# Performance work log

Measured on AMD Instinct MI355X. Metric: run time of the kernel, lower is better.

Reference implementation:

```python
import jax, jax.numpy as jnp
import numpy as np

DIM_IN = 16
DIM_OUT = 64

def setup_inputs() -> dict:
    key = jax.random.key(0)
    ks = jax.random.split(key, 7)
    B, T, N = 4, 8, 256
    s_in = 1.0 / np.sqrt(DIM_IN)
    s_out = 1.0 / np.sqrt(DIM_OUT)
    return {
        "query": jax.random.normal(ks[0], (B, N, DIM_IN), dtype=jnp.float32),
        "keys": jax.random.normal(ks[1], (B, T, N, DIM_IN), dtype=jnp.float32),
        "Wq": jax.random.uniform(ks[2], (DIM_IN, DIM_OUT), jnp.float32, -s_in, s_in),
        "bq": jax.random.uniform(ks[3], (DIM_OUT,), jnp.float32, -s_in, s_in),
        "Wk": jax.random.uniform(ks[4], (DIM_IN, DIM_OUT), jnp.float32, -s_in, s_in),
        "bk": jax.random.uniform(ks[5], (DIM_OUT,), jnp.float32, -s_in, s_in),
        "wt": jax.random.uniform(ks[6], (DIM_OUT,), jnp.float32, -s_out, s_out),
    }

def reference(query, keys, Wq, bq, Wk, bk, wt):
    # q: [B, N, D] -> [B, 1, N, 1, D]
    q = (jnp.einsum('bnf,fd->bnd', query, Wq) + bq)[:, None, :, None, :]
    # k: [B, T, N, D] -> [B, T, 1, N, D]
    k = (jnp.einsum('btnf,fd->btnd', keys, Wk) + bk)[:, :, None, :, :]
    # scores: [B, T, N, N] via tanh of broadcast add, reduced by wt
    scores = jnp.einsum('btnmd,d->btnm', jnp.tanh(q + k), wt)
    return jax.nn.softmax(scores, axis=-1)
```

## Files before the change

kernel.cpp:

```cpp
#include <hip/hip_runtime.h>

#define B_ 4
#define T_ 8
#define N_ 256
#define F_ 16
#define D_ 64
#define NP (D_/2)
#define CHUNK 8
#define NCH (N_/CHUNK)

#define SC 2.8853900817779268f
#define LOG2E 1.4426950408889634f

typedef __attribute__((ext_vector_type(16))) float f32x16;

__device__ __forceinline__ float fast_exp2(float x) { return __builtin_amdgcn_exp2f(x); }
__device__ __forceinline__ float fast_rcp(float x)  { return __builtin_amdgcn_rcpf(x); }

__global__ __launch_bounds__(256)
void tattn_proj_kernel(const float* __restrict__ query,
                       const float* __restrict__ keys,
                       const float* __restrict__ Wq, const float* __restrict__ bq,
                       const float* __restrict__ Wk, const float* __restrict__ bk,
                       float* __restrict__ Eq, float* __restrict__ Ek)
{
    const int tid = threadIdx.x;
    const int row = blockIdx.x * 4 + (tid >> 6);
    const int j   = tid & 63;
    const int NQ  = B_ * N_;

    if (row < NQ) {
        const float* in = query + (size_t)row * F_;
        float acc = bq[j];
        #pragma unroll
        for (int f = 0; f < F_; ++f) acc = fmaf(in[f], Wq[f * D_ + j], acc);
        Eq[(size_t)row * D_ + j] = fast_exp2(acc * SC);
    } else {
        const int r = row - NQ;
        const float* in = keys + (size_t)r * F_;
        float acc = bk[j];
        #pragma unroll
        for (int f = 0; f < F_; ++f) acc = fmaf(in[f], Wk[f * D_ + j], acc);
        Ek[(size_t)r * D_ + j] = fast_exp2(acc * SC);
    }
}

__global__ __launch_bounds__(256, 3)
void tattn_main_kernel(const float* __restrict__ Eq,
                       const float* __restrict__ Ek,
                       const float* __restrict__ wt,
                       float* __restrict__ out)
{
    __shared__ float pbuf[CHUNK][N_];
    __shared__ float wls[D_];
    __shared__ float totL[CHUNK];

    const int tid = threadIdx.x;
    const int bid = blockIdx.x;
    const int ch  = bid % NCH;
    const int t   = (bid / NCH) % T_;
    const int b   = bid / (NCH * T_);
    const int n0  = ch * CHUNK;

    if (tid < D_) wls[tid] = 2.0f * wt[tid];

    float kreg[D_];
    {
        const float* kp = Ek + (((size_t)(b * T_ + t)) * N_ + tid) * D_;
        #pragma unroll
        for (int d = 0; d < D_; d += 4) {
            float4 v = *reinterpret_cast<const float4*>(kp + d);
            kreg[d] = v.x; kreg[d+1] = v.y; kreg[d+2] = v.z; kreg[d+3] = v.w;
        }
    }
    __syncthreads();

    float wv[D_];
    #pragma unroll
    for (int d = 0; d < D_; d += 4) {
        float4 v = *reinterpret_cast<const float4*>(&wls[d]);
        wv[d] = v.x; wv[d+1] = v.y; wv[d+2] = v.z; wv[d+3] = v.w;
    }
    float Wsum = 0.f;
    #pragma unroll
    for (int d = 0; d < D_; ++d) Wsum += wv[d];
    Wsum *= 0.5f;

    const float* eqrow = Eq + ((size_t)(b * N_ + n0)) * D_;

    #pragma unroll 1
    for (int nn = 0; nn < CHUNK; ++nn) {
        f32x16 e0, e1, e2, e3;
        asm volatile("s_load_dwordx16 %0, %4, 0x0\n\t"
                     "s_load_dwordx16 %1, %4, 0x40\n\t"
                     "s_load_dwordx16 %2, %4, 0x80\n\t"
                     "s_load_dwordx16 %3, %4, 0xc0"
                     : "=&s"(e0), "=&s"(e1), "=&s"(e2), "=&s"(e3)
                     : "s"(eqrow));
        asm volatile("s_waitcnt lgkmcnt(0)"
                     : "+s"(e0), "+s"(e1), "+s"(e2), "+s"(e3));
        __builtin_amdgcn_sched_barrier(0);

        float a0 = 0.f, a1 = 0.f, a2 = 0.f, a3 = 0.f;
        #pragma unroll
        for (int pr = 0; pr < NP; ++pr) {
            float eqa, eqb;
            if      (pr <  8) { eqa = e0[2*pr];      eqb = e0[2*pr+1];      }
            else if (pr < 16) { eqa = e1[2*pr-16];   eqb = e1[2*pr-15];     }
            else if (pr < 24) { eqa = e2[2*pr-32];   eqb = e2[2*pr-31];     }
            else              { eqa = e3[2*pr-48];   eqb = e3[2*pr-47];     }
            float pA = fmaf(eqa, kreg[2*pr+0], 1.0f);
            float qA = fmaf(eqb, kreg[2*pr+1], 1.0f);
            float nA = fmaf(wv[2*pr+1], pA, wv[2*pr] * qA);
            float r  = fast_rcp(pA * qA);
            if      ((pr & 3) == 0) a0 = fmaf(nA, r, a0);
            else if ((pr & 3) == 1) a1 = fmaf(nA, r, a1);
            else if ((pr & 3) == 2) a2 = fmaf(nA, r, a2);
            else                    a3 = fmaf(nA, r, a3);
        }
        float score = Wsum - ((a0 + a1) + (a2 + a3));

        pbuf[nn][tid] = fast_exp2(score * LOG2E);
        eqrow += D_;
    }
    __syncthreads();

    const int lane = tid & 63;
    const int wid  = tid >> 6;
    #pragma unroll
    for (int rr = 0; rr < 2; ++rr) {
        const int row = wid * 2 + rr;
        float4 v = *reinterpret_cast<const float4*>(&pbuf[row][lane * 4]);
        float s = (v.x + v.y) + (v.z + v.w);
        #pragma unroll
        for (int off = 32; off >= 1; off >>= 1) s += __shfl_xor(s, off);
        if (lane == 0) totL[row] = s;
    }
    __syncthreads();

    const size_t obase = ((size_t)((b * T_ + t) * N_ + n0)) * N_ + tid;
    #pragma unroll
    for (int nn = 0; nn < CHUNK; ++nn)
        out[obase + (size_t)nn * N_] = pbuf[nn][tid] * fast_rcp(totL[nn]);
}

extern "C" void kernel_launch(void* const* d_in, const int* in_sizes, int n_in,
                              void* d_out, int out_size, void* d_ws, size_t ws_size,
                              hipStream_t stream) {
    const float* query = (const float*)d_in[0];
    const float* keys  = (const float*)d_in[1];
    const float* Wq    = (const float*)d_in[2];
    const float* bq    = (const float*)d_in[3];
    const float* Wk    = (const float*)d_in[4];
    const float* bk    = (const float*)d_in[5];
    const float* wt    = (const float*)d_in[6];
    float* out = (float*)d_out;

    float* Eq = (float*)d_ws;
    float* Ek = Eq + (size_t)B_ * N_ * D_;

    const int rows = B_ * N_ + B_ * T_ * N_;
    hipLaunchKernelGGL(tattn_proj_kernel, dim3(rows / 4), dim3(256), 0, stream,
                       query, keys, Wq, bq, Wk, bk, Eq, Ek);

    hipLaunchKernelGGL(tattn_main_kernel, dim3(B_ * T_ * NCH), dim3(256), 0, stream,
                       Eq, Ek, wt, out);
}
```

Measured before the change: 30.48 us.

## Fold wt weights into precomputed query stream and transpose key exponentials

```diff
diff --git a/kernel.cpp b/kernel.cpp
--- a/kernel.cpp
+++ b/kernel.cpp
@@ -22,7 +22,8 @@
                        const float* __restrict__ keys,
                        const float* __restrict__ Wq, const float* __restrict__ bq,
                        const float* __restrict__ Wk, const float* __restrict__ bk,
-                       float* __restrict__ Eq, float* __restrict__ Ek)
+                       const float* __restrict__ wt,
+                       float* __restrict__ StreamQ, float* __restrict__ EkT)
 {
     const int tid = threadIdx.x;
     const int row = blockIdx.x * 4 + (tid >> 6);
@@ -34,25 +35,35 @@
         float acc = bq[j];
         #pragma unroll
         for (int f = 0; f < F_; ++f) acc = fmaf(in[f], Wq[f * D_ + j], acc);
-        Eq[(size_t)row * D_ + j] = fast_exp2(acc * SC);
+        float eq = fast_exp2(acc * SC);
+        float wpart = wt[j ^ 1];
+        float* qs = StreamQ + (size_t)row * (4 * NP);
+        const int pr = j >> 1;
+        if ((j & 1) == 0) {
+            qs[4 * pr + 0] = eq;
+            qs[4 * pr + 2] = LOG2E * 2.0f * wpart * eq;
+        } else {
+            qs[4 * pr + 1] = eq;
+            qs[4 * pr + 3] = LOG2E * 2.0f * wpart * eq;
+        }
     } else {
-        const int r = row - NQ;
+        const int r  = row - NQ;
+        const int bt = r >> 8, n = r & (N_ - 1);
         const float* in = keys + (size_t)r * F_;
         float acc = bk[j];
         #pragma unroll
         for (int f = 0; f < F_; ++f) acc = fmaf(in[f], Wk[f * D_ + j], acc);
-        Ek[(size_t)r * D_ + j] = fast_exp2(acc * SC);
+        EkT[((size_t)bt * D_ + j) * N_ + n] = fast_exp2(acc * SC);
     }
 }
 
-__global__ __launch_bounds__(256, 3)
-void tattn_main_kernel(const float* __restrict__ Eq,
-                       const float* __restrict__ Ek,
+__global__ __launch_bounds__(256, 4)
+void tattn_main_kernel(const float* __restrict__ StreamQ,
+                       const float* __restrict__ EkT,
                        const float* __restrict__ wt,
                        float* __restrict__ out)
 {
     __shared__ float pbuf[CHUNK][N_];
-    __shared__ float wls[D_];
     __shared__ float totL[CHUNK];
 
     const int tid = threadIdx.x;
@@ -61,67 +72,78 @@
     const int t   = (bid / NCH) % T_;
     const int b   = bid / (NCH * T_);
     const int n0  = ch * CHUNK;
-
-    if (tid < D_) wls[tid] = 2.0f * wt[tid];
+    const int bt  = b * T_ + t;
 
     float kreg[D_];
     {
-        const float* kp = Ek + (((size_t)(b * T_ + t)) * N_ + tid) * D_;
+        const float* kp = EkT + (size_t)bt * D_ * N_ + tid;
         #pragma unroll
-        for (int d = 0; d < D_; d += 4) {
-            float4 v = *reinterpret_cast<const float4*>(kp + d);
-            kreg[d] = v.x; kreg[d+1] = v.y; kreg[d+2] = v.z; kreg[d+3] = v.w;
-        }
+        for (int d = 0; d < D_; ++d) kreg[d] = kp[(size_t)d * N_];
     }
-    __syncthreads();
 
-    float wv[D_];
-    #pragma unroll
-    for (int d = 0; d < D_; d += 4) {
-        float4 v = *reinterpret_cast<const float4*>(&wls[d]);
-        wv[d] = v.x; wv[d+1] = v.y; wv[d+2] = v.z; wv[d+3] = v.w;
-    }
+    float C01[NP];
     float Wsum = 0.f;
     #pragma unroll
-    for (int d = 0; d < D_; ++d) Wsum += wv[d];
-    Wsum *= 0.5f;
+    for (int pr = 0; pr < NP; ++pr) {
+        float w0 = wt[2 * pr], w1 = wt[2 * pr + 1];
+        C01[pr] = LOG2E * 2.0f * (w0 + w1);
+        Wsum += w0 + w1;
+    }
+    const float WsumL = Wsum * LOG2E;
 
-    const float* eqrow = Eq + ((size_t)(b * N_ + n0)) * D_;
+    const char* srow = (const char*)(StreamQ + ((size_t)(b * N_ + n0)) * (4 * NP));
+
+#define DO4(EV, PRB)                                                        \
+    {                                                                       \
+        _Pragma("unroll")                                                   \
+        for (int i = 0; i < 4; ++i) {                                       \
+            const int pr = (PRB) + i;                                       \
+            float eqa = EV[4*i+0], eqb = EV[4*i+1];                         \
+            float A   = EV[4*i+2], Bv  = EV[4*i+3];                         \
+            float pA = fmaf(eqa, kreg[2*pr+0], 1.0f);                       \
+            float qA = fmaf(eqb, kreg[2*pr+1], 1.0f);                       \
+            float nA = fmaf(A, kreg[2*pr+0], fmaf(Bv, kreg[2*pr+1], C01[pr])); \
+            float r  = fast_rcp(pA * qA);                                   \
+            if      ((pr & 3) == 0) a0 = fmaf(nA, r, a0);                   \
+            else if ((pr & 3) == 1) a1 = fmaf(nA, r, a1);                   \
+            else if ((pr & 3) == 2) a2 = fmaf(nA, r, a2);                   \
+            else                    a3 = fmaf(nA, r, a3);                   \
+        }                                                                   \
+    }
 
     #pragma unroll 1
     for (int nn = 0; nn < CHUNK; ++nn) {
-        f32x16 e0, e1, e2, e3;
-        asm volatile("s_load_dwordx16 %0, %4, 0x0\n\t"
-                     "s_load_dwordx16 %1, %4, 0x40\n\t"
-                     "s_load_dwordx16 %2, %4, 0x80\n\t"
-                     "s_load_dwordx16 %3, %4, 0xc0"
-                     : "=&s"(e0), "=&s"(e1), "=&s"(e2), "=&s"(e3)
-                     : "s"(eqrow));
-        asm volatile("s_waitcnt lgkmcnt(0)"
-                     : "+s"(e0), "+s"(e1), "+s"(e2), "+s"(e3));
-        __builtin_amdgcn_sched_barrier(0);
+        float a0 = 0.f, a1 = 0.f, a2 = 0.f, a3 = 0.f;
 
-        float a0 = 0.f, a1 = 0.f, a2 = 0.f, a3 = 0.f;
-        #pragma unroll
-        for (int pr = 0; pr < NP; ++pr) {
-            float eqa, eqb;
-            if      (pr <  8) { eqa = e0[2*pr];      eqb = e0[2*pr+1];      }
-            else if (pr < 16) { eqa = e1[2*pr-16];   eqb = e1[2*pr-15];     }
-            else if (pr < 24) { eqa = e2[2*pr-32];   eqb = e2[2*pr-31];     }
-            else              { eqa = e3[2*pr-48];   eqb = e3[2*pr-47];     }
-            float pA = fmaf(eqa, kreg[2*pr+0], 1.0f);
-            float qA = fmaf(eqb, kreg[2*pr+1], 1.0f);
-            float nA = fmaf(wv[2*pr+1], pA, wv[2*pr] * qA);
-            float r  = fast_rcp(pA * qA);
-            if      ((pr & 3) == 0) a0 = fmaf(nA, r, a0);
-            else if ((pr & 3) == 1) a1 = fmaf(nA, r, a1);
-            else if ((pr & 3) == 2) a2 = fmaf(nA, r, a2);
-            else                    a3 = fmaf(nA, r, a3);
+        {
+            f32x16 e0, e1, e2, e3;
+            asm volatile("s_load_dwordx16 %0, %4, 0x0\n\t"
+                         "s_load_dwordx16 %1, %4, 0x40\n\t"
+                         "s_load_dwordx16 %2, %4, 0x80\n\t"
+                         "s_load_dwordx16 %3, %4, 0xc0"
+                         : "=&s"(e0), "=&s"(e1), "=&s"(e2), "=&s"(e3)
+                         : "s"(srow));
+            asm volatile("s_waitcnt lgkmcnt(0)"
+                         : "+s"(e0), "+s"(e1), "+s"(e2), "+s"(e3));
+            __builtin_amdgcn_sched_barrier(0);
+            DO4(e0, 0) DO4(e1, 4) DO4(e2, 8) DO4(e3, 12)
         }
-        float score = Wsum - ((a0 + a1) + (a2 + a3));
+        {
+            f32x16 e0, e1, e2, e3;
+            asm volatile("s_load_dwordx16 %0, %4, 0x100\n\t"
+                         "s_load_dwordx16 %1, %4, 0x140\n\t"
+                         "s_load_dwordx16 %2, %4, 0x180\n\t"
+                         "s_load_dwordx16 %3, %4, 0x1c0"
+                         : "=&s"(e0), "=&s"(e1), "=&s"(e2), "=&s"(e3)
+                         : "s"(srow));
+            asm volatile("s_waitcnt lgkmcnt(0)"
+                         : "+s"(e0), "+s"(e1), "+s"(e2), "+s"(e3));
+            __builtin_amdgcn_sched_barrier(0);
+            DO4(e0, 16) DO4(e1, 20) DO4(e2, 24) DO4(e3, 28)
+        }
 
-        pbuf[nn][tid] = fast_exp2(score * LOG2E);
-        eqrow += D_;
+        pbuf[nn][tid] = fast_exp2(WsumL - ((a0 + a1) + (a2 + a3)));
+        srow += 4 * NP * sizeof(float);
     }
     __syncthreads();
 
@@ -138,10 +160,11 @@
     }
     __syncthreads();
 
-    const size_t obase = ((size_t)((b * T_ + t) * N_ + n0)) * N_ + tid;
+    const size_t obase = ((size_t)(bt * N_ + n0)) * N_ + tid;
     #pragma unroll
     for (int nn = 0; nn < CHUNK; ++nn)
         out[obase + (size_t)nn * N_] = pbuf[nn][tid] * fast_rcp(totL[nn]);
+#undef DO4
 }
 
 extern "C" void kernel_launch(void* const* d_in, const int* in_sizes, int n_in,
@@ -156,13 +179,13 @@
     const float* wt    = (const float*)d_in[6];
     float* out = (float*)d_out;
 
-    float* Eq = (float*)d_ws;
-    float* Ek = Eq + (size_t)B_ * N_ * D_;
+    float* StreamQ = (float*)d_ws;
+    float* EkT     = StreamQ + (size_t)B_ * N_ * 4 * NP;
 
     const int rows = B_ * N_ + B_ * T_ * N_;
     hipLaunchKernelGGL(tattn_proj_kernel, dim3(rows / 4), dim3(256), 0, stream,
-                       query, keys, Wq, bq, Wk, bk, Eq, Ek);
+                       query, keys, Wq, bq, Wk, bk, wt, StreamQ, EkT);
 
     hipLaunchKernelGGL(tattn_main_kernel, dim3(B_ * T_ * NCH), dim3(256), 0, stream,
-                       Eq, Ek, wt, out);
+                       StreamQ, EkT, wt, out);
 }
```

Result: slower. 94.61 us (+210.4%).
